# Kernel tuning notes

Measured on AMD Instinct MI355X. Metric: run time of the kernel, lower is better.

## Reference

```python
import jax, jax.numpy as jnp
import numpy as np

B, NQ, NK = 4, 384, 384
D_EQUI, D_QINV, D_KVINV = 64, 256, 256
D_MSG, D_FF, D_OUT = 64, 256, 64
IN_FEATS = 2 * D_MSG + D_EQUI + D_EQUI  # q_msg + k_msg + dotprods + dists


def setup_inputs() -> dict:
    key = jax.random.key(0)
    ks = jax.random.split(key, 12)
    inp = {
        "q_equi": jax.random.normal(ks[0], (B, NQ, 3, D_EQUI), jnp.float32),
        "q_inv": jax.random.normal(ks[1], (B, NQ, D_QINV), jnp.float32),
        "k_equi": jax.random.normal(ks[2], (B, NK, 3, D_EQUI), jnp.float32),
        "k_inv": jax.random.normal(ks[3], (B, NK, D_KVINV), jnp.float32),
        # q_message_proj / k_message_proj
        "Wq": jax.random.normal(ks[4], (D_QINV, D_MSG), jnp.float32) * 0.05,
        "bq": jax.random.normal(ks[5], (D_MSG,), jnp.float32) * 0.05,
        "Wk": jax.random.normal(ks[6], (D_KVINV, D_MSG), jnp.float32) * 0.05,
        "bk": jax.random.normal(ks[7], (D_MSG,), jnp.float32) * 0.05,
        # message_mlp: Linear(in_feats, d_ff) -> SiLU -> Linear(d_ff, d_out)
        "W1": jax.random.normal(ks[8], (IN_FEATS, D_FF), jnp.float32) * 0.05,
        "b1": jax.random.normal(ks[9], (D_FF,), jnp.float32) * 0.05,
        "W2": jax.random.normal(ks[10], (D_FF, D_OUT), jnp.float32) * 0.05,
        "b2": jax.random.normal(ks[11], (D_OUT,), jnp.float32) * 0.05,
    }
    return inp


def reference(q_equi, q_inv, k_equi, k_inv, Wq, bq, Wk, bk, W1, b1, W2, b2):
    Bq, Nq = q_inv.shape[:2]
    Nk = k_inv.shape[1]
    # per-channel dot products over the 3-dim coordinate axis: [B,Nq,Nk,d_equi]
    dotprods = jnp.einsum("bqce,bkce->bqke", q_equi, k_equi)
    # message projections broadcast across the pair grid
    q_msg = q_inv @ Wq + bq  # [B,Nq,d_msg]
    k_msg = k_inv @ Wk + bk  # [B,Nk,d_msg]
    q_msg_e = jnp.broadcast_to(q_msg[:, :, None, :], (Bq, Nq, Nk, q_msg.shape[-1]))
    k_msg_e = jnp.broadcast_to(k_msg[:, None, :, :], (Bq, Nq, Nk, k_msg.shape[-1]))
    # include_dists=True: per-channel Euclidean distance over the coord axis
    vec_dists = q_equi[:, :, None, :, :] - k_equi[:, None, :, :, :]  # [B,Nq,Nk,3,d_equi]
    dists = jnp.sqrt(jnp.sum(vec_dists * vec_dists, axis=3))  # [B,Nq,Nk,d_equi]
    pairwise_feats = jnp.concatenate([q_msg_e, k_msg_e, dotprods, dists], axis=-1)
    h = jax.nn.silu(pairwise_feats @ W1 + b1)
    return h @ W2 + b2
```

## Files before the change

kernel.cpp:

```cpp
#include <hip/hip_runtime.h>

typedef __bf16 bf16;
typedef float f32x4 __attribute__((ext_vector_type(4)));
typedef bf16 bf16x8 __attribute__((ext_vector_type(8)));
typedef bf16 bf16x4 __attribute__((ext_vector_type(4)));

#define NB 4
#define NQ 384
#define NK 384
#define DE 64
#define DQI 256
#define DFF 256
#define DMSG 64
#define DOUT 64

#define WS_AQT 0
#define WS_AKT 1572864
#define WS_W1T 3145728
#define WS_W2T 3211264

__global__ __launch_bounds__(256) void prep_kernel(
    const float* __restrict__ q_inv, const float* __restrict__ k_inv,
    const float* __restrict__ Wq, const float* __restrict__ bq,
    const float* __restrict__ Wk, const float* __restrict__ bk,
    const float* __restrict__ W1, const float* __restrict__ b1,
    const float* __restrict__ W2,
    float* __restrict__ AqT, float* __restrict__ AkT,
    bf16* __restrict__ w1t, bf16* __restrict__ w2t)
{
  const int t = threadIdx.x;
  const int bid = blockIdx.x;
  if (bid < 2 * NB * 24) {
    const bool isQ = bid < NB * 24;
    const int sub = isQ ? bid : bid - NB * 24;
    const int b = sub / 24, tile = sub % 24;
    const int n0 = tile * 16;
    __shared__ float sInv[16 * 256];
    __shared__ float sMsg[16 * 64];
    const float* inv = isQ ? q_inv : k_inv;
    const float* Wm = isQ ? Wq : Wk;
    const float* bm = isQ ? bq : bk;
#pragma unroll
    for (int r = 0; r < 16; ++r)
      sInv[r * 256 + t] = inv[(b * 384 + n0 + r) * 256 + t];
    __syncthreads();
    {
      const int e = t & 63, rq = t >> 6;
      float acc[4];
#pragma unroll
      for (int rr = 0; rr < 4; ++rr) acc[rr] = bm[e];
      for (int d = 0; d < 256; ++d) {
        float wv = Wm[d * DMSG + e];
#pragma unroll
        for (int rr = 0; rr < 4; ++rr) acc[rr] += sInv[(rq * 4 + rr) * 256 + d] * wv;
      }
#pragma unroll
      for (int rr = 0; rr < 4; ++rr) sMsg[(rq * 4 + rr) * 64 + e] = acc[rr];
    }
    __syncthreads();
    {
      const int c = t;
      const float* w1r = W1 + (isQ ? 0 : DMSG * DFF);
      float acc[16];
#pragma unroll
      for (int n = 0; n < 16; ++n) acc[n] = isQ ? b1[c] : 0.f;
      for (int e = 0; e < 64; ++e) {
        float wv = w1r[e * DFF + c];
#pragma unroll
        for (int n = 0; n < 16; ++n) acc[n] += sMsg[n * 64 + e] * wv;
      }
      float* dst = (isQ ? AqT : AkT) + (b * 256 + c) * 384 + n0;
#pragma unroll
      for (int n = 0; n < 16; ++n) dst[n] = acc[n];
    }
  } else if (bid == 2 * NB * 24) {
    const int cs = t;
    const int c = ((cs >> 5) << 5) + (((cs >> 4) & 1) << 2) + (((cs >> 2) & 3) << 3) + (cs & 3);
    for (int k8 = 0; k8 < 16; ++k8) {
      bf16x8 v;
#pragma unroll
      for (int j = 0; j < 8; ++j) {
        int k = k8 * 8 + j;
        v[j] = (bf16)W1[(128 + k) * DFF + c];
      }
      *(bf16x8*)&w1t[cs * 128 + k8 * 8] = v;
    }
  } else {
    const int ocol = t >> 2;
    const int ksc = t & 3;
    for (int k8 = 0; k8 < 8; ++k8) {
      bf16x8 v;
#pragma unroll
      for (int j = 0; j < 8; ++j) {
        int ks = ksc * 64 + k8 * 8 + j;
        int ct = ((ks >> 5) << 5) + (((ks >> 3) & 3) << 3) + (((ks >> 2) & 1) << 2) + (ks & 3);
        v[j] = (bf16)W2[ct * DOUT + ocol];
      }
      *(bf16x8*)&w2t[ocol * 256 + ksc * 64 + k8 * 8] = v;
    }
  }
}

__global__ __launch_bounds__(256, 2) void pair_kernel(
    const float* __restrict__ q_equi, const float* __restrict__ k_equi,
    const float* __restrict__ AqT, const float* __restrict__ AkT,
    const bf16* __restrict__ w1t, const bf16* __restrict__ w2t,
    const float* __restrict__ b2, float* __restrict__ out)
{
  __shared__ __align__(16) bf16 sA1[256 * 128];
  __shared__ __align__(16) bf16 sAb[16 * 4 * 16 * 8];

  const int t = threadIdx.x;
  const int bid = blockIdx.x;
  const int b = bid / (24 * 8);
  const int rem = bid % (24 * 8);
  const int qt = rem / 8, ks = rem % 8;
  const int q0 = qt * 16;
  const int k0b = ks * 48;

  const int lane = t & 63;
  const int w = t >> 6;
  const int r16 = lane & 15;
  const int g = lane >> 4;

  {
    const bf16* src = w1t + t * 128;
    bf16* dstrow = sA1 + t * 128;
#pragma unroll
    for (int k8 = 0; k8 < 16; ++k8)
      *(bf16x8*)&dstrow[((k8 ^ (t & 15)) << 3)] = *(const bf16x8*)&src[k8 * 8];
  }
  {
    const int c = ((t >> 5) << 5) + (((t >> 4) & 1) << 2) + (((t >> 2) & 3) << 3) + (t & 3);
    const float* aqp = AqT + (b * 256 + c) * 384 + q0;
    const int ct = t >> 4, rr = t & 15;
#pragma unroll
    for (int gg = 0; gg < 2; ++gg) {
      f32x4 v0 = *(const f32x4*)&aqp[gg * 8];
      f32x4 v1 = *(const f32x4*)&aqp[gg * 8 + 4];
      bf16x8 vv;
#pragma unroll
      for (int j = 0; j < 4; ++j) { vv[j] = (bf16)v0[j]; vv[4 + j] = (bf16)v1[j]; }
      *(bf16x8*)&sAb[((ct * 4 + gg) * 16 + rr) * 8] = vv;
    }
  }
  bf16x8 b1sel[4];
#pragma unroll
  for (int pt = 0; pt < 4; ++pt) {
#pragma unroll
    for (int j = 0; j < 8; ++j) {
      const int jj = g * 8 + j;
      float v;
      if (g < 2) v = (jj == r16) ? 1.f : 0.f;
      else v = ((jj - 16) == (w * 4 + pt)) ? 1.f : 0.f;
      b1sel[pt][j] = (bf16)v;
    }
  }

  for (int it = 0; it < 3; ++it) {
    const int k0i = k0b + it * 16;
    bf16x8 b1f[4][4];
    {
      const int qrow = b * NQ + q0 + r16;
      f32x4 qv[3][4];
#pragma unroll
      for (int c = 0; c < 3; ++c) {
        const float* qp = q_equi + (qrow * 3 + c) * DE;
        qv[c][0] = *(const f32x4*)&qp[g * 8];
        qv[c][1] = *(const f32x4*)&qp[g * 8 + 4];
        qv[c][2] = *(const f32x4*)&qp[32 + g * 8];
        qv[c][3] = *(const f32x4*)&qp[32 + g * 8 + 4];
      }
#pragma unroll
      for (int pt = 0; pt < 4; ++pt) {
        const int krow = b * NK + k0i + w * 4 + pt;
        f32x4 dt[4], s2[4];
#pragma unroll
        for (int h = 0; h < 4; ++h) { dt[h] = (f32x4){0,0,0,0}; s2[h] = (f32x4){0,0,0,0}; }
#pragma unroll
        for (int c = 0; c < 3; ++c) {
          const float* kp = k_equi + (krow * 3 + c) * DE;
          f32x4 kv0 = *(const f32x4*)&kp[g * 8];
          f32x4 kv1 = *(const f32x4*)&kp[g * 8 + 4];
          f32x4 kv2 = *(const f32x4*)&kp[32 + g * 8];
          f32x4 kv3 = *(const f32x4*)&kp[32 + g * 8 + 4];
          dt[0] += qv[c][0] * kv0; dt[1] += qv[c][1] * kv1;
          dt[2] += qv[c][2] * kv2; dt[3] += qv[c][3] * kv3;
          f32x4 e0 = qv[c][0] - kv0, e1 = qv[c][1] - kv1, e2 = qv[c][2] - kv2, e3 = qv[c][3] - kv3;
          s2[0] += e0 * e0; s2[1] += e1 * e1; s2[2] += e2 * e2; s2[3] += e3 * e3;
        }
        bf16x8 f0, f1, f2, f3;
#pragma unroll
        for (int j = 0; j < 4; ++j) {
          f0[j] = (bf16)dt[0][j]; f0[4 + j] = (bf16)dt[1][j];
          f1[j] = (bf16)dt[2][j]; f1[4 + j] = (bf16)dt[3][j];
          f2[j] = (bf16)__builtin_amdgcn_sqrtf(s2[0][j]);
          f2[4 + j] = (bf16)__builtin_amdgcn_sqrtf(s2[1][j]);
          f3[j] = (bf16)__builtin_amdgcn_sqrtf(s2[2][j]);
          f3[4 + j] = (bf16)__builtin_amdgcn_sqrtf(s2[3][j]);
        }
        b1f[pt][0] = f0; b1f[pt][1] = f1; b1f[pt][2] = f2; b1f[pt][3] = f3;
      }
    }
    {
      const int c = ((t >> 5) << 5) + (((t >> 4) & 1) << 2) + (((t >> 2) & 3) << 3) + (t & 3);
      const float* akp = AkT + (b * 256 + c) * 384 + k0i;
      const int ct = t >> 4, rr = t & 15;
#pragma unroll
      for (int gg = 2; gg < 4; ++gg) {
        f32x4 v0 = *(const f32x4*)&akp[(gg - 2) * 8];
        f32x4 v1 = *(const f32x4*)&akp[(gg - 2) * 8 + 4];
        bf16x8 vv;
#pragma unroll
        for (int j = 0; j < 4; ++j) { vv[j] = (bf16)v0[j]; vv[4 + j] = (bf16)v1[j]; }
        *(bf16x8*)&sAb[((ct * 4 + gg) * 16 + rr) * 8] = vv;
      }
    }
    __syncthreads();
    {
      f32x4 D2[4][4];
#pragma unroll
      for (int ot = 0; ot < 4; ++ot)
#pragma unroll
        for (int pt = 0; pt < 4; ++pt)
          D2[ot][pt] = (f32x4){0.f, 0.f, 0.f, 0.f};

#pragma unroll
      for (int kk2 = 0; kk2 < 8; ++kk2) {
        const int ctE = kk2 * 2, ctO = kk2 * 2 + 1;
        f32x4 dE[4], dO[4];
#pragma unroll
        for (int pt = 0; pt < 4; ++pt) {
          dE[pt] = (f32x4){0.f, 0.f, 0.f, 0.f};
          dO[pt] = (f32x4){0.f, 0.f, 0.f, 0.f};
        }
#pragma unroll
        for (int kk = 0; kk < 4; ++kk) {
          bf16x8 aE = *(const bf16x8*)&sA1[(ctE * 16 + r16) * 128 + (((kk * 4 + g) ^ r16) << 3)];
#pragma unroll
          for (int pt = 0; pt < 4; ++pt)
            dE[pt] = __builtin_amdgcn_mfma_f32_16x16x32_bf16(aE, b1f[pt][kk], dE[pt], 0, 0, 0);
          bf16x8 aO = *(const bf16x8*)&sA1[(ctO * 16 + r16) * 128 + (((kk * 4 + g) ^ r16) << 3)];
#pragma unroll
          for (int pt = 0; pt < 4; ++pt)
            dO[pt] = __builtin_amdgcn_mfma_f32_16x16x32_bf16(aO, b1f[pt][kk], dO[pt], 0, 0, 0);
        }
        {
          bf16x8 aBE = *(const bf16x8*)&sAb[((ctE * 4 + g) * 16 + r16) * 8];
          bf16x8 aBO = *(const bf16x8*)&sAb[((ctO * 4 + g) * 16 + r16) * 8];
#pragma unroll
          for (int pt = 0; pt < 4; ++pt) {
            dE[pt] = __builtin_amdgcn_mfma_f32_16x16x32_bf16(aBE, b1sel[pt], dE[pt], 0, 0, 0);
            dO[pt] = __builtin_amdgcn_mfma_f32_16x16x32_bf16(aBO, b1sel[pt], dO[pt], 0, 0, 0);
          }
        }
        bf16x8 a2[4];
#pragma unroll
        for (int ot = 0; ot < 4; ++ot)
          a2[ot] = *(const bf16x8*)&w2t[(ot * 16 + r16) * 256 + kk2 * 32 + g * 8];
#pragma unroll
        for (int pt = 0; pt < 4; ++pt) {
          bf16x8 b2f;
#pragma unroll
          for (int r = 0; r < 4; ++r) {
            float zE = dE[pt][r];
            float sE = zE * __builtin_amdgcn_rcpf(1.f + __builtin_amdgcn_exp2f(zE * -1.44269504f));
            b2f[r] = (bf16)sE;
            float zO = dO[pt][r];
            float sO = zO * __builtin_amdgcn_rcpf(1.f + __builtin_amdgcn_exp2f(zO * -1.44269504f));
            b2f[4 + r] = (bf16)sO;
          }
#pragma unroll
          for (int ot = 0; ot < 4; ++ot)
            D2[ot][pt] = __builtin_amdgcn_mfma_f32_16x16x32_bf16(a2[ot], b2f, D2[ot][pt], 0, 0, 0);
        }
      }
      f32x4 b2v[4];
#pragma unroll
      for (int ot = 0; ot < 4; ++ot)
        b2v[ot] = *(const f32x4*)&b2[ot * 16 + g * 4];
#pragma unroll
      for (int pt = 0; pt < 4; ++pt) {
        const int kg = k0i + w * 4 + pt;
        float* op = out + ((b * NQ + q0 + r16) * NK + kg) * 64 + g * 4;
#pragma unroll
        for (int ot = 0; ot < 4; ++ot) {
          f32x4 v = D2[ot][pt] + b2v[ot];
          *(f32x4*)&op[ot * 16] = v;
        }
      }
    }
    __syncthreads();
  }
}

extern "C" void kernel_launch(void* const* d_in, const int* in_sizes, int n_in,
                              void* d_out, int out_size, void* d_ws, size_t ws_size,
                              hipStream_t stream) {
  const float* q_equi = (const float*)d_in[0];
  const float* q_inv = (const float*)d_in[1];
  const float* k_equi = (const float*)d_in[2];
  const float* k_inv = (const float*)d_in[3];
  const float* Wq = (const float*)d_in[4];
  const float* bq = (const float*)d_in[5];
  const float* Wk = (const float*)d_in[6];
  const float* bk = (const float*)d_in[7];
  const float* W1 = (const float*)d_in[8];
  const float* b1 = (const float*)d_in[9];
  const float* W2 = (const float*)d_in[10];
  const float* b2 = (const float*)d_in[11];
  char* ws = (char*)d_ws;
  float* AqT = (float*)(ws + WS_AQT);
  float* AkT = (float*)(ws + WS_AKT);
  bf16* w1t = (bf16*)(ws + WS_W1T);
  bf16* w2t = (bf16*)(ws + WS_W2T);
  float* out = (float*)d_out;

  prep_kernel<<<2 * NB * 24 + 2, 256, 0, stream>>>(q_inv, k_inv, Wq, bq, Wk, bk, W1, b1, W2,
                                                   AqT, AkT, w1t, w2t);
  pair_kernel<<<NB * 24 * 8, 256, 0, stream>>>(q_equi, k_equi, AqT, AkT, w1t, w2t, b2, out);
}
```

Measured before the change: 352.5 us.

## Store projected q/k activations as pre-swizzled bf16 tiles and remap blocks

The prep kernel now writes the per-row W1 projections of q/k messages directly as bf16 in the exact tiled layout the pair kernel's shared-memory buffer uses. The pair kernel can then copy them with plain 16-byte loads instead of strided fp32 loads plus conversion, which halves workspace traffic. The change also remaps block indices so that blocks for different batches and q-tiles interleave, uses nontemporal stores for the large output, and drops the occupancy hint from launch bounds. The k-tile copy moves ahead of the geometric feature computation, and dropping the occupancy hint could change register allocation.

```diff
diff --git a/kernel.cpp b/kernel.cpp
--- a/kernel.cpp
+++ b/kernel.cpp
@@ -14,10 +14,10 @@
 #define DMSG 64
 #define DOUT 64
 
-#define WS_AQT 0
-#define WS_AKT 1572864
-#define WS_W1T 3145728
-#define WS_W2T 3211264
+#define WS_ABQ 0
+#define WS_ABK 786432
+#define WS_W1T 1572864
+#define WS_W2T 1638400
 
 __global__ __launch_bounds__(256) void prep_kernel(
     const float* __restrict__ q_inv, const float* __restrict__ k_inv,
@@ -25,7 +25,7 @@
     const float* __restrict__ Wk, const float* __restrict__ bk,
     const float* __restrict__ W1, const float* __restrict__ b1,
     const float* __restrict__ W2,
-    float* __restrict__ AqT, float* __restrict__ AkT,
+    bf16* __restrict__ Abq, bf16* __restrict__ Abk,
     bf16* __restrict__ w1t, bf16* __restrict__ w2t)
 {
   const int t = threadIdx.x;
@@ -69,9 +69,16 @@
 #pragma unroll
         for (int n = 0; n < 16; ++n) acc[n] += sMsg[n * 64 + e] * wv;
       }
-      float* dst = (isQ ? AqT : AkT) + (b * 256 + c) * 384 + n0;
-#pragma unroll
-      for (int n = 0; n < 16; ++n) dst[n] = acc[n];
+      const int cs = (c & 0xE0) | ((c & 0x18) >> 1) | ((c & 4) << 2) | (c & 3);
+      const int ct = cs >> 4, rr = cs & 15;
+      bf16* dst = (isQ ? Abq : Abk) + (b * 24 + tile) * 4096;
+#pragma unroll
+      for (int gg = 0; gg < 2; ++gg) {
+        bf16x8 vv;
+#pragma unroll
+        for (int j = 0; j < 8; ++j) vv[j] = (bf16)acc[gg * 8 + j];
+        *(bf16x8*)&dst[((ct * 2 + gg) * 16 + rr) * 8] = vv;
+      }
     }
   } else if (bid == 2 * NB * 24) {
     const int cs = t;
@@ -101,9 +108,9 @@
   }
 }
 
-__global__ __launch_bounds__(256, 2) void pair_kernel(
+__global__ __launch_bounds__(256) void pair_kernel(
     const float* __restrict__ q_equi, const float* __restrict__ k_equi,
-    const float* __restrict__ AqT, const float* __restrict__ AkT,
+    const bf16* __restrict__ Abq, const bf16* __restrict__ Abk,
     const bf16* __restrict__ w1t, const bf16* __restrict__ w2t,
     const float* __restrict__ b2, float* __restrict__ out)
 {
@@ -111,9 +118,10 @@
   __shared__ __align__(16) bf16 sAb[16 * 4 * 16 * 8];
 
   const int t = threadIdx.x;
-  const int bid = blockIdx.x;
-  const int b = bid / (24 * 8);
-  const int rem = bid % (24 * 8);
+  const int bid0 = blockIdx.x;
+  const int l = (bid0 & 7) * 96 + (bid0 >> 3);
+  const int b = l / 192;
+  const int rem = l % 192;
   const int qt = rem / 8, ks = rem % 8;
   const int q0 = qt * 16;
   const int k0b = ks * 48;
@@ -122,6 +130,7 @@
   const int w = t >> 6;
   const int r16 = lane & 15;
   const int g = lane >> 4;
+  const int ct = t >> 4, rr = t & 15;
 
   {
     const bf16* src = w1t + t * 128;
@@ -131,18 +140,11 @@
       *(bf16x8*)&dstrow[((k8 ^ (t & 15)) << 3)] = *(const bf16x8*)&src[k8 * 8];
   }
   {
-    const int c = ((t >> 5) << 5) + (((t >> 4) & 1) << 2) + (((t >> 2) & 3) << 3) + (t & 3);
-    const float* aqp = AqT + (b * 256 + c) * 384 + q0;
-    const int ct = t >> 4, rr = t & 15;
-#pragma unroll
-    for (int gg = 0; gg < 2; ++gg) {
-      f32x4 v0 = *(const f32x4*)&aqp[gg * 8];
-      f32x4 v1 = *(const f32x4*)&aqp[gg * 8 + 4];
-      bf16x8 vv;
-#pragma unroll
-      for (int j = 0; j < 4; ++j) { vv[j] = (bf16)v0[j]; vv[4 + j] = (bf16)v1[j]; }
-      *(bf16x8*)&sAb[((ct * 4 + gg) * 16 + rr) * 8] = vv;
-    }
+    const bf16* src = Abq + (b * 24 + qt) * 4096;
+#pragma unroll
+    for (int gg = 0; gg < 2; ++gg)
+      *(bf16x8*)&sAb[((ct * 4 + gg) * 16 + rr) * 8] =
+          *(const bf16x8*)&src[((ct * 2 + gg) * 16 + rr) * 8];
   }
   bf16x8 b1sel[4];
 #pragma unroll
@@ -159,6 +161,13 @@
 
   for (int it = 0; it < 3; ++it) {
     const int k0i = k0b + it * 16;
+    {
+      const bf16* src = Abk + (b * 24 + (k0i >> 4)) * 4096;
+#pragma unroll
+      for (int gg = 0; gg < 2; ++gg)
+        *(bf16x8*)&sAb[((ct * 4 + 2 + gg) * 16 + rr) * 8] =
+            *(const bf16x8*)&src[((ct * 2 + gg) * 16 + rr) * 8];
+    }
     bf16x8 b1f[4][4];
     {
       const int qrow = b * NQ + q0 + r16;
@@ -202,20 +211,6 @@
         b1f[pt][0] = f0; b1f[pt][1] = f1; b1f[pt][2] = f2; b1f[pt][3] = f3;
       }
     }
-    {
-      const int c = ((t >> 5) << 5) + (((t >> 4) & 1) << 2) + (((t >> 2) & 3) << 3) + (t & 3);
-      const float* akp = AkT + (b * 256 + c) * 384 + k0i;
-      const int ct = t >> 4, rr = t & 15;
-#pragma unroll
-      for (int gg = 2; gg < 4; ++gg) {
-        f32x4 v0 = *(const f32x4*)&akp[(gg - 2) * 8];
-        f32x4 v1 = *(const f32x4*)&akp[(gg - 2) * 8 + 4];
-        bf16x8 vv;
-#pragma unroll
-        for (int j = 0; j < 4; ++j) { vv[j] = (bf16)v0[j]; vv[4 + j] = (bf16)v1[j]; }
-        *(bf16x8*)&sAb[((ct * 4 + gg) * 16 + rr) * 8] = vv;
-      }
-    }
     __syncthreads();
     {
       f32x4 D2[4][4];
@@ -286,7 +281,7 @@
 #pragma unroll
         for (int ot = 0; ot < 4; ++ot) {
           f32x4 v = D2[ot][pt] + b2v[ot];
-          *(f32x4*)&op[ot * 16] = v;
+          __builtin_nontemporal_store(v, (f32x4*)&op[ot * 16]);
         }
       }
     }
@@ -310,13 +305,13 @@
   const float* W2 = (const float*)d_in[10];
   const float* b2 = (const float*)d_in[11];
   char* ws = (char*)d_ws;
-  float* AqT = (float*)(ws + WS_AQT);
-  float* AkT = (float*)(ws + WS_AKT);
+  bf16* Abq = (bf16*)(ws + WS_ABQ);
+  bf16* Abk = (bf16*)(ws + WS_ABK);
   bf16* w1t = (bf16*)(ws + WS_W1T);
   bf16* w2t = (bf16*)(ws + WS_W2T);
   float* out = (float*)d_out;
 
   prep_kernel<<<2 * NB * 24 + 2, 256, 0, stream>>>(q_inv, k_inv, Wq, bq, Wk, bk, W1, b1, W2,
-                                                   AqT, AkT, w1t, w2t);
-  pair_kernel<<<NB * 24 * 8, 256, 0, stream>>>(q_equi, k_equi, AqT, AkT, w1t, w2t, b2, out);
+                                                   Abq, Abk, w1t, w2t);
+  pair_kernel<<<NB * 24 * 8, 256, 0, stream>>>(q_equi, k_equi, Abq, Abk, w1t, w2t, b2, out);
 }
```

New measurement: 340.5 us. 3.4% less time.
